# Kernel tuning notes

Hardware: AMD Instinct MI355X
Metric: run time of the kernel (lower is better)

## Reference

```python
import jax, jax.numpy as jnp
import numpy as np


def setup_inputs() -> dict:
    key = jax.random.key(0)
    k1, k2 = jax.random.split(key)
    n_nodes, n_feat, n_edges = 100000, 64, 1600000
    x = jax.random.normal(k1, (n_nodes, n_feat), dtype=jnp.float32)
    edge_index = jax.random.randint(k2, (2, n_edges), 0, n_nodes, dtype=jnp.int64)
    return {"x": x, "edge_index": edge_index}


def reference(x, edge_index):
    # Faithful JAX version of OneHopGCNNormNodeLabelAggregator.forward:
    #   adj = SparseTensor.from_edge_index(edge_index)  (values = 1)
    #   adj_norm = gcn_norm(adj)  -> add self-loops (diag=1), symmetric D^-1/2 A D^-1/2
    #   x_neighbors = adj_norm.t() @ x
    n = x.shape[0]
    self_loops = jnp.arange(n, dtype=edge_index.dtype)
    row = jnp.concatenate([edge_index[0], self_loops])  # source of adj entry A[row, col]
    col = jnp.concatenate([edge_index[1], self_loops])
    # degree over rows (sparsesum dim=1 after fill_diag)
    deg = jax.ops.segment_sum(jnp.ones(row.shape, x.dtype), row, num_segments=n)
    deg_inv_sqrt = jnp.where(deg > 0, jax.lax.rsqrt(deg), 0.0).astype(x.dtype)
    # symmetric norm weight per edge
    w = deg_inv_sqrt[row] * deg_inv_sqrt[col]  # [E+n]
    # adj_norm.t() @ x : out[col] += w * x[row]
    x_neighbors = jax.ops.segment_sum(w[:, None] * x[row], col, num_segments=n)
    return x_neighbors
```

## Files before the change

### kernel.cpp

```cpp
#include <hip/hip_runtime.h>

#define NFEAT 64
#define BSHIFT 8
#define BCOLS 256
#define NBMAX 512
#define CAP 5120
#define CHUNK 4096
#define PT 512
#define NITP (CHUNK / PT)
#define FT 512
#define FBIT (CAP / FT)


__device__ __forceinline__ unsigned short f2bf(float f) {
    unsigned int u = __float_as_uint(f);
    return (unsigned short)((u + 0x7FFFu + ((u >> 16) & 1u)) >> 16);
}

__device__ __forceinline__ float bflo(unsigned int u) {
    return __uint_as_float(u << 16);
}
__device__ __forceinline__ float bfhi(unsigned int u) {
    return __uint_as_float(u & 0xFFFF0000u);
}

__device__ __forceinline__ int wave_incl_scan(int v, int lane) {
    #pragma unroll
    for (int off = 1; off < 64; off <<= 1) {
        int u = __shfl_up(v, off);
        if (lane >= off) v += u;
    }
    return v;
}

__global__ void k_init(int* __restrict__ bcur, int* __restrict__ bcurR) {
    int t = threadIdx.x;
    bcur[t]  = t * CAP;
    bcurR[t] = t * CAP;
}

__global__ __launch_bounds__(PT)
void k_partCR(const int* __restrict__ rows, const int* __restrict__ cols,
              int* __restrict__ bcur, int* __restrict__ bcurR,
              int* __restrict__ part, unsigned char* __restrict__ partR, int E) {
    __shared__ int histC[NBMAX];
    __shared__ int histR[NBMAX];
    __shared__ int gbaseC[NBMAX];
    __shared__ int gbaseR[NBMAX];
    __shared__ int wsumC[8];
    __shared__ int wsumR[8];
    __shared__ int stageC[CHUNK];
    __shared__ unsigned char stageR[CHUNK];
    __shared__ unsigned short bidC[CHUNK];
    __shared__ unsigned short bidR[CHUNK];
    int chunk0 = blockIdx.x * CHUNK;
    int cnt = min(CHUNK, E - chunk0);
    int t = threadIdx.x;
    int lane = t & 63, wid = t >> 6;

    histC[t] = 0; histR[t] = 0;
    __syncthreads();

    int pk[NITP];
    unsigned char rpk[NITP];
    unsigned short cb[NITP], rb[NITP];
    #pragma unroll
    for (int k = 0; k < NITP; k++) {
        int i = t + k * PT;
        if (i < cnt) {
            int c = cols[chunk0 + i];
            int r = rows[chunk0 + i];
            int b  = c >> BSHIFT;
            int b2 = r >> BSHIFT;
            pk[k]  = ((c & (BCOLS - 1)) << 17) | r;
            rpk[k] = (unsigned char)(r & (BCOLS - 1));
            cb[k] = (unsigned short)b;
            rb[k] = (unsigned short)b2;
            atomicAdd(&histC[b], 1);
            atomicAdd(&histR[b2], 1);
        }
    }
    __syncthreads();

    int v1 = histC[t];
    int inc1 = wave_incl_scan(v1, lane);
    if (lane == 63) wsumC[wid] = inc1;
    int v2 = histR[t];
    int inc2 = wave_incl_scan(v2, lane);
    if (lane == 63) wsumR[wid] = inc2;
    __syncthreads();
    int addC = 0, addR = 0;
    #pragma unroll
    for (int k = 0; k < 8; k++) {
        if (k < wid) { addC += wsumC[k]; addR += wsumR[k]; }
    }
    int exC = inc1 - v1 + addC;
    int exR = inc2 - v2 + addR;
    gbaseC[t] = (v1 > 0) ? (atomicAdd(&bcur[t], v1) - exC) : 0;
    gbaseR[t] = (v2 > 0) ? (atomicAdd(&bcurR[t], v2) - exR) : 0;
    histC[t] = exC;
    histR[t] = exR;
    __syncthreads();

    #pragma unroll
    for (int k = 0; k < NITP; k++) {
        int i = t + k * PT;
        if (i < cnt) {
            int p = atomicAdd(&histC[cb[k]], 1);
            stageC[p] = pk[k];
            bidC[p] = cb[k];
            int p2 = atomicAdd(&histR[rb[k]], 1);
            stageR[p2] = rpk[k];
            bidR[p2] = rb[k];
        }
    }
    __syncthreads();
    for (int p = t; p < cnt; p += PT) {
        int b = bidC[p];
        int idx = gbaseC[b] + p;
        if (idx < (b + 1) * CAP) part[idx] = stageC[p];
        int b2 = bidR[p];
        int idx2 = gbaseR[b2] + p;
        if (idx2 < (b2 + 1) * CAP) partR[idx2] = stageR[p];
    }
}

__global__ __launch_bounds__(FT)
void k_fill(const unsigned char* __restrict__ partR, const int* __restrict__ bcurR,
            int* __restrict__ part, const int* __restrict__ bcur,
            const float4* __restrict__ x4, float* __restrict__ dinv,
            ushort4* __restrict__ xs4, int* __restrict__ ptr,
            int* __restrict__ ptr2, int n) {
    __shared__ int lcnt[BCOLS];
    __shared__ float ldinv[BCOLS];
    __shared__ int cur[BCOLS];
    __shared__ int wsum[4];
    __shared__ int stage[CAP];
    int b = blockIdx.x;
    int s = b * CAP;
    int t = threadIdx.x;
    int lane = t & 63, wid = t >> 6;

    int cntR = min(bcurR[b] - s, CAP);
    if (t < BCOLS) lcnt[t] = 0;
    __syncthreads();
    for (int i = t; i < cntR; i += FT)
        atomicAdd(&lcnt[partR[s + i]], 1);
    __syncthreads();
    if (t < BCOLS) {
        float d = rsqrtf((float)(lcnt[t] + 1));
        ldinv[t] = d;
        int gr = (b << BSHIFT) + t;
        if (gr < n) dinv[gr] = d;
    }
    __syncthreads();
    size_t base4 = (size_t)(b << BSHIFT) << 4;
    int lim = min(BCOLS, n - (b << BSHIFT)) << 4;
    for (int i = t; i < lim; i += FT) {
        float dd = ldinv[i >> 4];
        float4 vv = x4[base4 + i];
        ushort4 o;
        o.x = f2bf(dd * vv.x); o.y = f2bf(dd * vv.y);
        o.z = f2bf(dd * vv.z); o.w = f2bf(dd * vv.w);
        xs4[base4 + i] = o;
    }

    int cntC = min(bcur[b] - s, CAP);
    __syncthreads();
    if (t < BCOLS) lcnt[t] = 0;
    __syncthreads();

    int pk[FBIT];
    #pragma unroll
    for (int k = 0; k < FBIT; k++) {
        int i = t + k * FT;
        if (i < cntC) {
            int v2 = part[s + i];
            pk[k] = v2;
            atomicAdd(&lcnt[v2 >> 17], 1);
        }
    }
    __syncthreads();

    int v = 0, inc = 0;
    if (t < BCOLS) {
        v = lcnt[t];
        inc = wave_incl_scan(v, lane);
        if (lane == 63) wsum[wid] = inc;
    }
    __syncthreads();
    if (t < BCOLS) {
        int add = 0;
        if (wid > 0) add += wsum[0];
        if (wid > 1) add += wsum[1];
        if (wid > 2) add += wsum[2];
        int ex = inc - v + add;
        cur[t] = ex;
        int c = (b << BSHIFT) + t;
        if (c < n) { ptr[c] = s + ex; ptr2[c] = s + ex + v; }
    }
    __syncthreads();

    #pragma unroll
    for (int k = 0; k < FBIT; k++) {
        int i = t + k * FT;
        if (i < cntC) {
            int v2 = pk[k];
            int p = atomicAdd(&cur[v2 >> 17], 1);
            stage[p] = v2 & 0x1FFFF;
        }
    }
    __syncthreads();
    for (int p = t; p < cntC; p += FT) part[s + p] = stage[p];
}

__global__ void k_gather(const unsigned short* __restrict__ xs,
                         const float* __restrict__ dinv,
                         const int* __restrict__ ptr, const int* __restrict__ ptr2,
                         const int* __restrict__ csr,
                         float4* __restrict__ out4, int n) {
    int node = blockIdx.x * 4 + (threadIdx.x >> 6);
    if (node >= n) return;
    int lane = threadIdx.x & 63;
    int g  = lane >> 3;
    int li = lane & 7;
    int s = ptr[node], e = ptr2[node];
    float a0 = 0.f, a1 = 0.f, a2 = 0.f, a3 = 0.f;
    float a4 = 0.f, a5 = 0.f, a6 = 0.f, a7 = 0.f;
    for (int base = s; base < e; base += 64) {
        int m = e - base; if (m > 64) m = 64;
        int idx = base + ((lane < m) ? lane : (m - 1));
        int myr = csr[idx];
        int mr = (m + 7) & ~7;
        int j = 0;
        for (; j + 16 <= mr; j += 16) {
            int rA = __shfl(myr, j + g);
            int rB = __shfl(myr, j + 8 + g);
            float vA = (j + g < m) ? 1.0f : 0.0f;
            float vB = (j + 8 + g < m) ? 1.0f : 0.0f;
            uint4 uA = *((const uint4*)(xs + ((size_t)rA << 6)) + li);
            uint4 uB = *((const uint4*)(xs + ((size_t)rB << 6)) + li);
            a0 += vA * bflo(uA.x); a1 += vA * bfhi(uA.x);
            a2 += vA * bflo(uA.y); a3 += vA * bfhi(uA.y);
            a4 += vA * bflo(uA.z); a5 += vA * bfhi(uA.z);
            a6 += vA * bflo(uA.w); a7 += vA * bfhi(uA.w);
            a0 += vB * bflo(uB.x); a1 += vB * bfhi(uB.x);
            a2 += vB * bflo(uB.y); a3 += vB * bfhi(uB.y);
            a4 += vB * bflo(uB.z); a5 += vB * bfhi(uB.z);
            a6 += vB * bflo(uB.w); a7 += vB * bfhi(uB.w);
        }
        for (; j < mr; j += 8) {
            int r = __shfl(myr, j + g);
            float val = (j + g < m) ? 1.0f : 0.0f;
            uint4 u = *((const uint4*)(xs + ((size_t)r << 6)) + li);
            a0 += val * bflo(u.x); a1 += val * bfhi(u.x);
            a2 += val * bflo(u.y); a3 += val * bfhi(u.y);
            a4 += val * bflo(u.z); a5 += val * bfhi(u.z);
            a6 += val * bflo(u.w); a7 += val * bfhi(u.w);
        }
    }
    a0 += __shfl_xor(a0, 8);  a1 += __shfl_xor(a1, 8);
    a2 += __shfl_xor(a2, 8);  a3 += __shfl_xor(a3, 8);
    a4 += __shfl_xor(a4, 8);  a5 += __shfl_xor(a5, 8);
    a6 += __shfl_xor(a6, 8);  a7 += __shfl_xor(a7, 8);
    a0 += __shfl_xor(a0, 16); a1 += __shfl_xor(a1, 16);
    a2 += __shfl_xor(a2, 16); a3 += __shfl_xor(a3, 16);
    a4 += __shfl_xor(a4, 16); a5 += __shfl_xor(a5, 16);
    a6 += __shfl_xor(a6, 16); a7 += __shfl_xor(a7, 16);
    a0 += __shfl_xor(a0, 32); a1 += __shfl_xor(a1, 32);
    a2 += __shfl_xor(a2, 32); a3 += __shfl_xor(a3, 32);
    a4 += __shfl_xor(a4, 32); a5 += __shfl_xor(a5, 32);
    a6 += __shfl_xor(a6, 32); a7 += __shfl_xor(a7, 32);
    if (lane < 8) {
        float dc = dinv[node];
        uint4 us = *((const uint4*)(xs + ((size_t)node << 6)) + li);
        size_t ob = ((size_t)node << 4) + (li << 1);
        float4 r0, r1;
        r0.x = dc * (a0 + bflo(us.x));
        r0.y = dc * (a1 + bfhi(us.x));
        r0.z = dc * (a2 + bflo(us.y));
        r0.w = dc * (a3 + bfhi(us.y));
        r1.x = dc * (a4 + bflo(us.z));
        r1.y = dc * (a5 + bfhi(us.z));
        r1.z = dc * (a6 + bflo(us.w));
        r1.w = dc * (a7 + bfhi(us.w));
        out4[ob] = r0;
        out4[ob + 1] = r1;
    }
}

extern "C" void kernel_launch(void* const* d_in, const int* in_sizes, int n_in,
                              void* d_out, int out_size, void* d_ws, size_t ws_size,
                              hipStream_t stream) {
    const float* x    = (const float*)d_in[0];
    const int*   eidx = (const int*)d_in[1];

    const int n = in_sizes[0] / NFEAT;
    const int E = in_sizes[1] / 2;
    const int* rows = eidx;
    const int* cols = eidx + E;
    float* out = (float*)d_out;

    const int nbuck = (n + BCOLS - 1) >> BSHIFT;

    char* w = (char*)d_ws;
    int*   bcur  = (int*)w;     w += NBMAX * 4;
    int*   bcurR = (int*)w;     w += NBMAX * 4;
    int*   ptr   = (int*)w;     w += (size_t)n * 4;
    int*   ptr2  = (int*)w;     w += (size_t)n * 4;
    float* dinv  = (float*)w;   w += (size_t)n * 4;
    w = (char*)(((uintptr_t)w + 15) & ~(uintptr_t)15);
    unsigned short* xs = (unsigned short*)w;  w += (size_t)n * NFEAT * 2;
    int*   part  = (int*)w;     w += (size_t)nbuck * CAP * 4;
    unsigned char* partR = (unsigned char*)w;
    int*   csr   = part;

    k_init<<<1, NBMAX, 0, stream>>>(bcur, bcurR);

    int nchunk = (E + CHUNK - 1) / CHUNK;
    k_partCR<<<nchunk, PT, 0, stream>>>(rows, cols, bcur, bcurR, part, partR, E);
    k_fill<<<nbuck, FT, 0, stream>>>(partR, bcurR, part, bcur, (const float4*)x,
                                     dinv, (ushort4*)xs, ptr, ptr2, n);

    k_gather<<<(n + 3) / 4, 256, 0, stream>>>(xs, dinv, ptr, ptr2, csr,
                                              (float4*)out, n);
}
```

Measured before the change: 149.5 us.

## Fuse column-bucket sort with neighbor gather, keeping the CSR in shared memory

The column counting sort moves out of the fill kernel into a new fused kernel. That kernel sorts each 256-column bucket into shared memory and then gathers neighbor rows straight from the shared stage array. This removes the global CSR write-back, the ptr/ptr2 arrays and a separate gather launch. The gather now gives 8 lanes per node with a two-deep software-pipelined load loop, but only nbuck (~391) blocks of 512 threads run it. That is far fewer blocks than before and may cause poor latency hiding and load imbalance on a gather-bound workload.

```diff
diff --git a/kernel.cpp b/kernel.cpp
--- a/kernel.cpp
+++ b/kernel.cpp
@@ -9,7 +9,8 @@
 #define PT 512
 #define NITP (CHUNK / PT)
 #define FT 512
-#define FBIT (CAP / FT)
+#define UT 512
+#define FBIT (CAP / UT)
 
 
 __device__ __forceinline__ unsigned short f2bf(float f) {
@@ -126,20 +127,14 @@
 }
 
 __global__ __launch_bounds__(FT)
-void k_fill(const unsigned char* __restrict__ partR, const int* __restrict__ bcurR,
-            int* __restrict__ part, const int* __restrict__ bcur,
-            const float4* __restrict__ x4, float* __restrict__ dinv,
-            ushort4* __restrict__ xs4, int* __restrict__ ptr,
-            int* __restrict__ ptr2, int n) {
+void k_fillR(const unsigned char* __restrict__ partR, const int* __restrict__ bcurR,
+             const float4* __restrict__ x4, float* __restrict__ dinv,
+             ushort4* __restrict__ xs4, int n) {
     __shared__ int lcnt[BCOLS];
     __shared__ float ldinv[BCOLS];
-    __shared__ int cur[BCOLS];
-    __shared__ int wsum[4];
-    __shared__ int stage[CAP];
     int b = blockIdx.x;
     int s = b * CAP;
     int t = threadIdx.x;
-    int lane = t & 63, wid = t >> 6;
 
     int cntR = min(bcurR[b] - s, CAP);
     if (t < BCOLS) lcnt[t] = 0;
@@ -164,17 +159,32 @@
         o.z = f2bf(dd * vv.z); o.w = f2bf(dd * vv.w);
         xs4[base4 + i] = o;
     }
-
-    int cntC = min(bcur[b] - s, CAP);
-    __syncthreads();
+}
+
+__global__ __launch_bounds__(UT)
+void k_fuse(const int* __restrict__ part, const int* __restrict__ bcur,
+            const unsigned short* __restrict__ xs,
+            const float* __restrict__ dinv,
+            float4* __restrict__ out4, int n) {
+    __shared__ int lcnt[BCOLS];
+    __shared__ int lps[BCOLS];
+    __shared__ int cur[BCOLS];
+    __shared__ int wsum[4];
+    __shared__ int stage[CAP];
+    int b = blockIdx.x;
+    int s = b * CAP;
+    int cnt = min(bcur[b] - s, CAP);
+    int t = threadIdx.x;
+    int lane = t & 63, wid = t >> 6;
+
     if (t < BCOLS) lcnt[t] = 0;
     __syncthreads();
 
     int pk[FBIT];
     #pragma unroll
     for (int k = 0; k < FBIT; k++) {
-        int i = t + k * FT;
-        if (i < cntC) {
+        int i = t + k * UT;
+        if (i < cnt) {
             int v2 = part[s + i];
             pk[k] = v2;
             atomicAdd(&lcnt[v2 >> 17], 1);
@@ -195,97 +205,87 @@
         if (wid > 1) add += wsum[1];
         if (wid > 2) add += wsum[2];
         int ex = inc - v + add;
+        lps[t] = ex;
         cur[t] = ex;
-        int c = (b << BSHIFT) + t;
-        if (c < n) { ptr[c] = s + ex; ptr2[c] = s + ex + v; }
     }
     __syncthreads();
 
     #pragma unroll
     for (int k = 0; k < FBIT; k++) {
-        int i = t + k * FT;
-        if (i < cntC) {
+        int i = t + k * UT;
+        if (i < cnt) {
             int v2 = pk[k];
             int p = atomicAdd(&cur[v2 >> 17], 1);
             stage[p] = v2 & 0x1FFFF;
         }
     }
     __syncthreads();
-    for (int p = t; p < cntC; p += FT) part[s + p] = stage[p];
-}
-
-__global__ void k_gather(const unsigned short* __restrict__ xs,
-                         const float* __restrict__ dinv,
-                         const int* __restrict__ ptr, const int* __restrict__ ptr2,
-                         const int* __restrict__ csr,
-                         float4* __restrict__ out4, int n) {
-    int node = blockIdx.x * 4 + (threadIdx.x >> 6);
-    if (node >= n) return;
-    int lane = threadIdx.x & 63;
-    int g  = lane >> 3;
-    int li = lane & 7;
-    int s = ptr[node], e = ptr2[node];
-    float a0 = 0.f, a1 = 0.f, a2 = 0.f, a3 = 0.f;
-    float a4 = 0.f, a5 = 0.f, a6 = 0.f, a7 = 0.f;
-    for (int base = s; base < e; base += 64) {
-        int m = e - base; if (m > 64) m = 64;
-        int idx = base + ((lane < m) ? lane : (m - 1));
-        int myr = csr[idx];
-        int mr = (m + 7) & ~7;
-        int j = 0;
-        for (; j + 16 <= mr; j += 16) {
-            int rA = __shfl(myr, j + g);
-            int rB = __shfl(myr, j + 8 + g);
-            float vA = (j + g < m) ? 1.0f : 0.0f;
-            float vB = (j + 8 + g < m) ? 1.0f : 0.0f;
-            uint4 uA = *((const uint4*)(xs + ((size_t)rA << 6)) + li);
-            uint4 uB = *((const uint4*)(xs + ((size_t)rB << 6)) + li);
-            a0 += vA * bflo(uA.x); a1 += vA * bfhi(uA.x);
-            a2 += vA * bflo(uA.y); a3 += vA * bfhi(uA.y);
-            a4 += vA * bflo(uA.z); a5 += vA * bfhi(uA.z);
-            a6 += vA * bflo(uA.w); a7 += vA * bfhi(uA.w);
-            a0 += vB * bflo(uB.x); a1 += vB * bfhi(uB.x);
-            a2 += vB * bflo(uB.y); a3 += vB * bfhi(uB.y);
-            a4 += vB * bflo(uB.z); a5 += vB * bfhi(uB.z);
-            a6 += vB * bflo(uB.w); a7 += vB * bfhi(uB.w);
-        }
-        for (; j < mr; j += 8) {
-            int r = __shfl(myr, j + g);
-            float val = (j + g < m) ? 1.0f : 0.0f;
-            uint4 u = *((const uint4*)(xs + ((size_t)r << 6)) + li);
-            a0 += val * bflo(u.x); a1 += val * bfhi(u.x);
-            a2 += val * bflo(u.y); a3 += val * bfhi(u.y);
-            a4 += val * bflo(u.z); a5 += val * bfhi(u.z);
-            a6 += val * bflo(u.w); a7 += val * bfhi(u.w);
-        }
-    }
-    a0 += __shfl_xor(a0, 8);  a1 += __shfl_xor(a1, 8);
-    a2 += __shfl_xor(a2, 8);  a3 += __shfl_xor(a3, 8);
-    a4 += __shfl_xor(a4, 8);  a5 += __shfl_xor(a5, 8);
-    a6 += __shfl_xor(a6, 8);  a7 += __shfl_xor(a7, 8);
-    a0 += __shfl_xor(a0, 16); a1 += __shfl_xor(a1, 16);
-    a2 += __shfl_xor(a2, 16); a3 += __shfl_xor(a3, 16);
-    a4 += __shfl_xor(a4, 16); a5 += __shfl_xor(a5, 16);
-    a6 += __shfl_xor(a6, 16); a7 += __shfl_xor(a7, 16);
-    a0 += __shfl_xor(a0, 32); a1 += __shfl_xor(a1, 32);
-    a2 += __shfl_xor(a2, 32); a3 += __shfl_xor(a3, 32);
-    a4 += __shfl_xor(a4, 32); a5 += __shfl_xor(a5, 32);
-    a6 += __shfl_xor(a6, 32); a7 += __shfl_xor(a7, 32);
-    if (lane < 8) {
-        float dc = dinv[node];
-        uint4 us = *((const uint4*)(xs + ((size_t)node << 6)) + li);
-        size_t ob = ((size_t)node << 4) + (li << 1);
-        float4 r0, r1;
-        r0.x = dc * (a0 + bflo(us.x));
-        r0.y = dc * (a1 + bfhi(us.x));
-        r0.z = dc * (a2 + bflo(us.y));
-        r0.w = dc * (a3 + bfhi(us.y));
-        r1.x = dc * (a4 + bflo(us.z));
-        r1.y = dc * (a5 + bfhi(us.z));
-        r1.z = dc * (a6 + bflo(us.w));
-        r1.w = dc * (a7 + bfhi(us.w));
-        out4[ob] = r0;
-        out4[ob + 1] = r1;
+
+    int gg = t >> 3, li = t & 7;
+    #pragma unroll
+    for (int cc = 0; cc < BCOLS; cc += 64) {
+        int c = cc + gg;
+        int node = (b << BSHIFT) + c;
+        if (node < n) {
+            int ss = lps[c];
+            int len = lcnt[c];
+            float a0 = 0.f, a1 = 0.f, a2 = 0.f, a3 = 0.f;
+            float a4 = 0.f, a5 = 0.f, a6 = 0.f, a7 = 0.f;
+            int npair = len >> 1;
+            uint4 u0, u1;
+            if (npair > 0) {
+                int r0 = stage[ss], r1 = stage[ss + 1];
+                u0 = *((const uint4*)(xs + ((size_t)r0 << 6)) + li);
+                u1 = *((const uint4*)(xs + ((size_t)r1 << 6)) + li);
+            }
+            for (int q = 1; q < npair; q++) {
+                int p = ss + q * 2;
+                int r0 = stage[p], r1 = stage[p + 1];
+                uint4 n0 = *((const uint4*)(xs + ((size_t)r0 << 6)) + li);
+                uint4 n1 = *((const uint4*)(xs + ((size_t)r1 << 6)) + li);
+                a0 += bflo(u0.x); a1 += bfhi(u0.x);
+                a2 += bflo(u0.y); a3 += bfhi(u0.y);
+                a4 += bflo(u0.z); a5 += bfhi(u0.z);
+                a6 += bflo(u0.w); a7 += bfhi(u0.w);
+                a0 += bflo(u1.x); a1 += bfhi(u1.x);
+                a2 += bflo(u1.y); a3 += bfhi(u1.y);
+                a4 += bflo(u1.z); a5 += bfhi(u1.z);
+                a6 += bflo(u1.w); a7 += bfhi(u1.w);
+                u0 = n0; u1 = n1;
+            }
+            if (npair > 0) {
+                a0 += bflo(u0.x); a1 += bfhi(u0.x);
+                a2 += bflo(u0.y); a3 += bfhi(u0.y);
+                a4 += bflo(u0.z); a5 += bfhi(u0.z);
+                a6 += bflo(u0.w); a7 += bfhi(u0.w);
+                a0 += bflo(u1.x); a1 += bfhi(u1.x);
+                a2 += bflo(u1.y); a3 += bfhi(u1.y);
+                a4 += bflo(u1.z); a5 += bfhi(u1.z);
+                a6 += bflo(u1.w); a7 += bfhi(u1.w);
+            }
+            if (len & 1) {
+                int r = stage[ss + len - 1];
+                uint4 u = *((const uint4*)(xs + ((size_t)r << 6)) + li);
+                a0 += bflo(u.x); a1 += bfhi(u.x);
+                a2 += bflo(u.y); a3 += bfhi(u.y);
+                a4 += bflo(u.z); a5 += bfhi(u.z);
+                a6 += bflo(u.w); a7 += bfhi(u.w);
+            }
+            float dc = dinv[node];
+            uint4 us = *((const uint4*)(xs + ((size_t)node << 6)) + li);
+            float4 r0o, r1o;
+            r0o.x = dc * (a0 + bflo(us.x));
+            r0o.y = dc * (a1 + bfhi(us.x));
+            r0o.z = dc * (a2 + bflo(us.y));
+            r0o.w = dc * (a3 + bfhi(us.y));
+            r1o.x = dc * (a4 + bflo(us.z));
+            r1o.y = dc * (a5 + bfhi(us.z));
+            r1o.z = dc * (a6 + bflo(us.w));
+            r1o.w = dc * (a7 + bfhi(us.w));
+            size_t ob = ((size_t)node << 4) + (li << 1);
+            out4[ob] = r0o;
+            out4[ob + 1] = r1o;
+        }
     }
 }
 
@@ -306,22 +306,18 @@
     char* w = (char*)d_ws;
     int*   bcur  = (int*)w;     w += NBMAX * 4;
     int*   bcurR = (int*)w;     w += NBMAX * 4;
-    int*   ptr   = (int*)w;     w += (size_t)n * 4;
-    int*   ptr2  = (int*)w;     w += (size_t)n * 4;
     float* dinv  = (float*)w;   w += (size_t)n * 4;
     w = (char*)(((uintptr_t)w + 15) & ~(uintptr_t)15);
     unsigned short* xs = (unsigned short*)w;  w += (size_t)n * NFEAT * 2;
     int*   part  = (int*)w;     w += (size_t)nbuck * CAP * 4;
     unsigned char* partR = (unsigned char*)w;
-    int*   csr   = part;
 
     k_init<<<1, NBMAX, 0, stream>>>(bcur, bcurR);
 
     int nchunk = (E + CHUNK - 1) / CHUNK;
     k_partCR<<<nchunk, PT, 0, stream>>>(rows, cols, bcur, bcurR, part, partR, E);
-    k_fill<<<nbuck, FT, 0, stream>>>(partR, bcurR, part, bcur, (const float4*)x,
-                                     dinv, (ushort4*)xs, ptr, ptr2, n);
-
-    k_gather<<<(n + 3) / 4, 256, 0, stream>>>(xs, dinv, ptr, ptr2, csr,
-                                              (float4*)out, n);
-}
+    k_fillR<<<nbuck, FT, 0, stream>>>(partR, bcurR, (const float4*)x,
+                                      dinv, (ushort4*)xs, n);
+    k_fuse<<<nbuck, UT, 0, stream>>>(part, bcur, xs, dinv,
+                                     (float4*)out, n);
+}
```

Measured after the change: 140.5 us. -6.0%, faster.
